# Optimization experiments

Hardware: AMD Instinct MI355X
Metric: run time of the kernel (lower is better)

## Reference

```python
import jax, jax.numpy as jnp
import numpy as np
import math

# ---- static hyperparameters (match init_kwargs) ----
B, N = 128, 2048          # batch, latent tokens per item
IN_DIM, HID = 256, 128    # router input / hidden width
R, MP = 8, 4              # num VQ experts, num phy modes
K, D = 256, 64            # codebook size, code dim
K_BITS = 8                # ceil(log2(K))
BPS = 4                   # bits per symbol -> 16-QAM
MQ = 1 << BPS             # constellation size
TAU = 1.0                 # router temperature
VQ_T = 0.5                # VQ soft-assignment temperature
BIT_T = 0.5               # bit-space mixture temperature
LN_EPS = 1e-5


def _int_to_bits_np(n, num_bits):
    # MSB-first bits of 0..n-1, shape [n, num_bits], float32
    shifts = np.arange(num_bits - 1, -1, -1)
    return ((np.arange(n)[:, None] >> shifts) & 1).astype(np.float32)


def _qam_constellation_np(M):
    # square QAM normalized to max power 1 (matches qam_constellation)
    s = int(math.sqrt(M))
    levels = np.arange(-(s - 1), s + 1, 2).astype(np.float32)
    xs, ys = np.meshgrid(levels, levels, indexing='ij')
    pts = np.stack([xs.reshape(-1), ys.reshape(-1)], axis=-1)
    max_p = (pts ** 2).sum(-1).max()
    return (pts / np.sqrt(max_p + 1e-9)).astype(np.float32)


LABEL_BITS = jnp.asarray(_int_to_bits_np(K, K_BITS))   # [K, 8] identity labeling
CAND_BITS = jnp.asarray(_int_to_bits_np(MQ, BPS))      # [16, 4]
CONST = jnp.asarray(_qam_constellation_np(MQ))         # [16, 2]
POWER = jnp.asarray(np.array([0.25, 0.5, 0.75, 1.0], dtype=np.float32))  # per phy mode


def setup_inputs() -> dict:
    key = jax.random.key(0)
    ks = jax.random.split(key, 10)
    s = 0.02
    return {
        'phi': jax.random.normal(ks[0], (B, IN_DIM), jnp.float32),
        'z': jax.random.normal(ks[1], (B, N, D), jnp.float32),
        'ln_gamma': jnp.ones((IN_DIM,), jnp.float32),
        'ln_beta': jnp.zeros((IN_DIM,), jnp.float32),
        'W1': jax.random.normal(ks[2], (IN_DIM, HID), jnp.float32) * s,
        'b1': jnp.zeros((HID,), jnp.float32),
        'W2': jax.random.normal(ks[3], (HID, HID), jnp.float32) * s,
        'b2': jnp.zeros((HID,), jnp.float32),
        'We': jax.random.normal(ks[4], (HID, R), jnp.float32) * s,
        'be': jnp.zeros((R,), jnp.float32),
        'Wm': jax.random.normal(ks[5], (HID, MP), jnp.float32) * s,
        'bm': jnp.zeros((MP,), jnp.float32),
        'codebooks': jax.random.normal(ks[6], (R, K, D), jnp.float32) * s,
    }


def reference(phi, z, ln_gamma, ln_beta, W1, b1, W2, b2, We, be, Wm, bm, codebooks):
    # ---- ModeRouter: LayerNorm -> MLP(GELU) -> expert/phy heads ----
    mu = phi.mean(-1, keepdims=True)
    var = ((phi - mu) ** 2).mean(-1, keepdims=True)
    x = (phi - mu) * jax.lax.rsqrt(var + LN_EPS) * ln_gamma + ln_beta
    h = jax.nn.gelu(x @ W1 + b1, approximate=False)
    h = jax.nn.gelu(h @ W2 + b2, approximate=False)
    logits_e = h @ We + be                      # [B, R]
    logits_m = h @ Wm + bm                      # [B, MP]
    p_m = jax.nn.softmax(logits_m / TAU, axis=-1)

    # ---- hard expert selection -> per-sample codebook gather ----
    expert_idx = jnp.argmax(logits_e, axis=-1)  # [B]
    cb = codebooks[expert_idx]                  # [B, K, D]

    # ---- VQ distances + soft assignment (dominant memory traffic) ----
    d = (jnp.sum(z ** 2, -1, keepdims=True)
         - 2.0 * jnp.einsum('bnd,bkd->bnk', z, cb)
         + jnp.sum(cb ** 2, -1)[:, None, :])    # [B, N, K]
    soft_assign = jax.nn.softmax(-d / VQ_T, axis=-1)

    # ---- soft code labels -> soft bits -> symbols ----
    soft_bits = jnp.einsum('bnk,kc->bnc', soft_assign, LABEL_BITS)  # [B, N, 8]
    sb = soft_bits.reshape(B, N * K_BITS // BPS, BPS)               # [B, S, 4]
    dist = jnp.sum((sb[..., None, :] - CAND_BITS) ** 2, -1)         # [B, S, 16]
    w_sym = jax.nn.softmax(-dist / BIT_T, axis=-1)
    x_sym = jnp.einsum('bsm,mc->bsc', w_sym, CONST)                 # [B, S, 2]

    # ---- soft phy-mode power blending ----
    scale = p_m @ POWER                                             # [B]
    return x_sym * scale[:, None, None]
```

## Files before the change

kernel.cpp:

```cpp
#include <hip/hip_runtime.h>

typedef __bf16 bf16;
typedef bf16 bf16x8 __attribute__((ext_vector_type(8)));
typedef float f32x4 __attribute__((ext_vector_type(4)));

#define NB    128
#define NTOK  2048
#define INDIM 256
#define HIDW  128
#define NEXP  8
#define NMODE 4
#define KC    256
#define DC    64
#define NSYM  4096
#define TPBK  2

#define RLN2_4 5.770780163555853f
#define RLN2_2 2.8853900817779268f
#define NLN2_8 0.0866433975699932f

__global__ __launch_bounds__(256)
void router_kernel(const float* __restrict__ phi,
                   const float* __restrict__ ln_g, const float* __restrict__ ln_b,
                   const float* __restrict__ W1, const float* __restrict__ b1,
                   const float* __restrict__ W2, const float* __restrict__ b2,
                   const float* __restrict__ We, const float* __restrict__ be,
                   const float* __restrict__ Wm, const float* __restrict__ bm,
                   float* __restrict__ scale_out, int* __restrict__ eidx_out)
{
  const int b = blockIdx.x, t = threadIdx.x;
  __shared__ double xs[INDIM];
  __shared__ double hs[HIDW];
  __shared__ double part[2][HIDW];
  __shared__ double red4[4];
  __shared__ double lg[NEXP + NMODE];

  double v = (double)phi[b * INDIM + t];
  double s = v;
  #pragma unroll
  for (int off = 32; off; off >>= 1) s += __shfl_down(s, off);
  if ((t & 63) == 0) red4[t >> 6] = s;
  __syncthreads();
  double mu = (red4[0] + red4[1] + red4[2] + red4[3]) * (1.0 / 256.0);
  double dv = v - mu;
  double s2 = dv * dv;
  #pragma unroll
  for (int off = 32; off; off >>= 1) s2 += __shfl_down(s2, off);
  __syncthreads();
  if ((t & 63) == 0) red4[t >> 6] = s2;
  __syncthreads();
  double var = (red4[0] + red4[1] + red4[2] + red4[3]) * (1.0 / 256.0);
  xs[t] = dv * (1.0 / sqrt(var + 1e-5)) * (double)ln_g[t] + (double)ln_b[t];
  __syncthreads();

  const int n = t & 127, h = t >> 7;

  {
    double a0 = 0.0, a1 = 0.0;
    const int i0 = h * 128;
    #pragma unroll 4
    for (int i = 0; i < 128; i += 2) {
      a0 += xs[i0 + i]     * (double)W1[(i0 + i)     * HIDW + n];
      a1 += xs[i0 + i + 1] * (double)W1[(i0 + i + 1) * HIDW + n];
    }
    part[h][n] = a0 + a1;
  }
  __syncthreads();
  if (h == 0) {
    double a = part[0][n] + part[1][n] + (double)b1[n];
    hs[n] = a * 0.5 * (1.0 + erf(a * 0.70710678118654752440));
  }
  __syncthreads();

  {
    double a0 = 0.0, a1 = 0.0;
    const int i0 = h * 64;
    #pragma unroll 4
    for (int i = 0; i < 64; i += 2) {
      a0 += hs[i0 + i]     * (double)W2[(i0 + i)     * HIDW + n];
      a1 += hs[i0 + i + 1] * (double)W2[(i0 + i + 1) * HIDW + n];
    }
    part[h][n] = a0 + a1;
  }
  __syncthreads();
  double h2v = 0.0;
  if (h == 0) {
    double a = part[0][n] + part[1][n] + (double)b2[n];
    h2v = a * 0.5 * (1.0 + erf(a * 0.70710678118654752440));
  }
  __syncthreads();
  if (h == 0) part[0][n] = h2v;
  __syncthreads();

  if (t < 192) {
    const int g = t >> 4, j = t & 15;
    const float* W; int stride, col; double bias;
    if (g < NEXP) { W = We; stride = NEXP;  col = g;        bias = (double)be[g]; }
    else          { W = Wm; stride = NMODE; col = g - NEXP; bias = (double)bm[g - NEXP]; }
    double a = 0.0;
    #pragma unroll
    for (int i = 0; i < 8; ++i)
      a += part[0][j * 8 + i] * (double)W[(j * 8 + i) * stride + col];
    a += __shfl_down(a, 8);
    a += __shfl_down(a, 4);
    a += __shfl_down(a, 2);
    a += __shfl_down(a, 1);
    if (j == 0) lg[g] = a + bias;
  }
  __syncthreads();
  if (t == 0) {
    int best = 0; double bv = lg[0];
    for (int j = 1; j < NEXP; ++j) if (lg[j] > bv) { bv = lg[j]; best = j; }
    eidx_out[b] = best;
    double m = lg[NEXP];
    for (int j = 1; j < NMODE; ++j) m = fmax(m, lg[NEXP + j]);
    double den = 0.0, num = 0.0;
    for (int j = 0; j < NMODE; ++j) {
      double e = exp(lg[NEXP + j] - m);
      den += e; num += e * (0.25 * (j + 1));
    }
    scale_out[b] = (float)(num / den);
  }
}

__global__ __launch_bounds__(256, 3)
void vq_kernel(const float* __restrict__ z, const float* __restrict__ codebooks,
               const float* __restrict__ scale_arr, const int* __restrict__ eidx,
               float* __restrict__ out)
{
  __shared__ __align__(16) bf16 cb_s[KC * DC];
  __shared__ float cn2h_s[KC];
  __shared__ __align__(16) float sb_s[4][32 * 8];

  const int blk  = blockIdx.x;
  const int b    = blk >> 3;
  const int tg   = blk & 7;
  const int tid  = threadIdx.x;
  const int lane = tid & 63;
  const int wid  = tid >> 6;
  const int q    = lane >> 4;
  const int c    = lane & 15;

  {
    const int e = eidx[b];
    const float* __restrict__ src = codebooks + (size_t)e * KC * DC + tid * DC;
    char* dstrow = (char*)cb_s + tid * 128;
    const int sw = tid & 7;
    float nrm = 0.f;
    #pragma unroll
    for (int j = 0; j < 8; ++j) {
      float4 va = *(const float4*)(src + j * 8);
      float4 vb = *(const float4*)(src + j * 8 + 4);
      bf16x8 p;
      p[0] = (bf16)(va.x * RLN2_4); p[1] = (bf16)(va.y * RLN2_4);
      p[2] = (bf16)(va.z * RLN2_4); p[3] = (bf16)(va.w * RLN2_4);
      p[4] = (bf16)(vb.x * RLN2_4); p[5] = (bf16)(vb.y * RLN2_4);
      p[6] = (bf16)(vb.z * RLN2_4); p[7] = (bf16)(vb.w * RLN2_4);
      #pragma unroll
      for (int u = 0; u < 8; ++u) { float f = (float)p[u]; nrm += f * f; }
      *(bf16x8*)(dstrow + ((j ^ sw) * 16)) = p;
    }
    cn2h_s[tid] = -NLN2_8 * nrm;
  }
  const float scale_b = scale_arr[b];
  __syncthreads();

  const char* pa0 = (const char*)cb_s + c * 128 + ((q    ) ^ (c & 7)) * 16;
  const char* pa1 = (const char*)cb_s + c * 128 + ((q + 4) ^ (c & 7)) * 16;
  const float* __restrict__ cn2q = cn2h_s + q * 4;

  for (int tile = 0; tile < TPBK; ++tile) {
    const int tokw = tg * (TPBK * 128) + tile * 128 + wid * 32;

    bf16x8 zb[2][2];
    #pragma unroll
    for (int nt = 0; nt < 2; ++nt) {
      const float* __restrict__ zt = z + ((size_t)b * NTOK + tokw + nt * 16 + c) * DC + q * 8;
      #pragma unroll
      for (int ks = 0; ks < 2; ++ks) {
        float4 va = *(const float4*)(zt + ks * 32);
        float4 vb = *(const float4*)(zt + ks * 32 + 4);
        bf16x8 p;
        p[0] = (bf16)va.x; p[1] = (bf16)va.y; p[2] = (bf16)va.z; p[3] = (bf16)va.w;
        p[4] = (bf16)vb.x; p[5] = (bf16)vb.y; p[6] = (bf16)vb.z; p[7] = (bf16)vb.w;
        zb[nt][ks] = p;
      }
    }

    float E[2]  = {0.f, 0.f}, S0[2] = {0.f, 0.f}, S1[2] = {0.f, 0.f},
          S2[2] = {0.f, 0.f}, S3[2] = {0.f, 0.f}, R0[2] = {0.f, 0.f}, R1[2] = {0.f, 0.f};
    #pragma unroll
    for (int cc = 0; cc < 4; ++cc) {
      #pragma unroll
      for (int ci = 0; ci < 4; ++ci) {
        const int ct = cc * 4 + ci;
        f32x4 cinit = *(const f32x4*)(cn2q + ct * 16);
        bf16x8 a0 = *(const bf16x8*)(pa0 + ct * 2048);
        bf16x8 a1 = *(const bf16x8*)(pa1 + ct * 2048);
        #pragma unroll
        for (int nt = 0; nt < 2; ++nt) {
          f32x4 a = __builtin_amdgcn_mfma_f32_16x16x32_bf16(a0, zb[nt][0], cinit, 0, 0, 0);
          a = __builtin_amdgcn_mfma_f32_16x16x32_bf16(a1, zb[nt][1], a, 0, 0, 0);
          float e0 = __builtin_amdgcn_exp2f(a[0]);
          float e1 = __builtin_amdgcn_exp2f(a[1]);
          float e2 = __builtin_amdgcn_exp2f(a[2]);
          float e3 = __builtin_amdgcn_exp2f(a[3]);
          float s01 = e0 + e1, s23 = e2 + e3, g = s01 + s23;
          E[nt] += g; R0[nt] += s23; R1[nt] += e1 + e3;
          if (ct & 8) S0[nt] += g;
          if (ct & 4) S1[nt] += g;
          if (ct & 2) S2[nt] += g;
          if (ct & 1) S3[nt] += g;
        }
      }
      __builtin_amdgcn_sched_barrier(0);
    }

    #pragma unroll
    for (int nt = 0; nt < 2; ++nt) {
      float En = E[nt];
      float Ep = En + __shfl_xor(En, 16);
      float B5 = En + __shfl_xor(En, 32);
      float Et = Ep + __shfl_xor(Ep, 32);
      float s0 = S0[nt], s1 = S1[nt], s2 = S2[nt], s3 = S3[nt], r0 = R0[nt], r1 = R1[nt];
      #define BF2(x) x += __shfl_xor(x, 16); x += __shfl_xor(x, 32);
      BF2(s0) BF2(s1) BF2(s2) BF2(s3) BF2(r0) BF2(r1)
      #undef BF2
      const float rinv = __builtin_amdgcn_rcpf(Et);

      float* row = &sb_s[wid][(nt * 16 + c) * 8];
      float v1 = (q == 0) ? s0 : (q == 1) ? s1 : (q == 2) ? s2 : s3;
      float v2 = (q == 0) ? r0 : (q == 1) ? B5 : (q == 2) ? Ep : r1;
      const int p2 = (q == 3) ? 7 : (6 - q);
      row[q]  = v1 * rinv;
      row[p2] = v2 * rinv;
    }

    {
      const int tok = lane >> 1, sym = lane & 1;
      const float* sb = &sb_s[wid][tok * 8 + sym * 4];
      float u0 = sb[0], u1 = sb[1], u2 = sb[2], u3 = sb[3];
      float wsum = 0.f, xa = 0.f, ya = 0.f;
      #pragma unroll
      for (int m = 0; m < 16; ++m) {
        float su = 0.f;
        if (m & 8) su += u0;
        if (m & 4) su += u1;
        if (m & 2) su += u2;
        if (m & 1) su += u3;
        const float pc = (float)__builtin_popcount(m);
        float ev = __builtin_amdgcn_exp2f(su * RLN2_4 - pc * RLN2_2);
        wsum += ev;
        xa += ev * (float)(2 * (m >> 2) - 3);
        ya += ev * (float)(2 * (m & 3) - 3);
      }
      const float fac = scale_b * 0.23570226039551584f * __builtin_amdgcn_rcpf(wsum);
      const int nidx = tokw + tok;
      float2* op = (float2*)(out + (((size_t)b * NSYM) + 2 * (size_t)nidx + sym) * 2);
      *op = make_float2(xa * fac, ya * fac);
    }
  }
}

extern "C" void kernel_launch(void* const* d_in, const int* in_sizes, int n_in,
                              void* d_out, int out_size, void* d_ws, size_t ws_size,
                              hipStream_t stream) {
  const float* phi  = (const float*)d_in[0];
  const float* z    = (const float*)d_in[1];
  const float* ln_g = (const float*)d_in[2];
  const float* ln_b = (const float*)d_in[3];
  const float* W1   = (const float*)d_in[4];
  const float* b1   = (const float*)d_in[5];
  const float* W2   = (const float*)d_in[6];
  const float* b2   = (const float*)d_in[7];
  const float* We   = (const float*)d_in[8];
  const float* be   = (const float*)d_in[9];
  const float* Wm   = (const float*)d_in[10];
  const float* bm   = (const float*)d_in[11];
  const float* cbk  = (const float*)d_in[12];
  float* out   = (float*)d_out;
  float* scale = (float*)d_ws;
  int*   eidx  = (int*)((char*)d_ws + 512);

  router_kernel<<<NB, 256, 0, stream>>>(phi, ln_g, ln_b, W1, b1, W2, b2,
                                        We, be, Wm, bm, scale, eidx);
  vq_kernel<<<NB * 8, 256, 0, stream>>>(z, cbk, scale, eidx, out);
}
```

Measured before the change: 143.1 us.

## Stage codebook in two halves to halve LDS and double VQ grid

The VQ kernel now holds only half of the codebook (128 codes) in shared memory at a time. It sweeps the first half, syncs, restages the second half, and sweeps again, with the bit-0 accumulation driven by which half is loaded. Each block handles one 128-token tile instead of two, and the grid grows from 1024 to 2048 blocks. The aim is lower LDS use per block, so more blocks fit per CU and there is more parallelism. The cost is that each block stages the codebook from global memory, converts it and syncs twice, and total codebook staging work per batch doubles.

```diff
diff --git a/kernel.cpp b/kernel.cpp
--- a/kernel.cpp
+++ b/kernel.cpp
@@ -11,9 +11,9 @@
 #define NEXP  8
 #define NMODE 4
 #define KC    256
+#define KH    128
 #define DC    64
 #define NSYM  4096
-#define TPBK  2
 
 #define RLN2_4 5.770780163555853f
 #define RLN2_2 2.8853900817779268f
@@ -123,142 +123,161 @@
   }
 }
 
+__device__ __forceinline__ void stage_half(int half, int tid, int e,
+                                           const float* __restrict__ codebooks,
+                                           bf16* cb_s, float* cn2h_s)
+{
+  const int code = tid >> 1, prt = tid & 1;
+  const float* __restrict__ src = codebooks + (size_t)e * KC * DC
+                                + (size_t)(half * KH + code) * DC + prt * 32;
+  char* dstrow = (char*)cb_s + code * 128;
+  const int sw = code & 7;
+  float nrm = 0.f;
+  #pragma unroll
+  for (int j2 = 0; j2 < 4; ++j2) {
+    const int j = prt * 4 + j2;
+    float4 va = *(const float4*)(src + j2 * 8);
+    float4 vb = *(const float4*)(src + j2 * 8 + 4);
+    bf16x8 p;
+    p[0] = (bf16)(va.x * RLN2_4); p[1] = (bf16)(va.y * RLN2_4);
+    p[2] = (bf16)(va.z * RLN2_4); p[3] = (bf16)(va.w * RLN2_4);
+    p[4] = (bf16)(vb.x * RLN2_4); p[5] = (bf16)(vb.y * RLN2_4);
+    p[6] = (bf16)(vb.z * RLN2_4); p[7] = (bf16)(vb.w * RLN2_4);
+    #pragma unroll
+    for (int u = 0; u < 8; ++u) { float f = (float)p[u]; nrm += f * f; }
+    *(bf16x8*)(dstrow + ((j ^ sw) * 16)) = p;
+  }
+  nrm += __shfl_xor(nrm, 1);
+  if (prt == 0) cn2h_s[code] = -NLN2_8 * nrm;
+}
+
 __global__ __launch_bounds__(256, 3)
 void vq_kernel(const float* __restrict__ z, const float* __restrict__ codebooks,
                const float* __restrict__ scale_arr, const int* __restrict__ eidx,
                float* __restrict__ out)
 {
-  __shared__ __align__(16) bf16 cb_s[KC * DC];
-  __shared__ float cn2h_s[KC];
+  __shared__ __align__(16) bf16 cb_s[KH * DC];
+  __shared__ float cn2h_s[KH];
   __shared__ __align__(16) float sb_s[4][32 * 8];
 
   const int blk  = blockIdx.x;
-  const int b    = blk >> 3;
-  const int tg   = blk & 7;
+  const int b    = blk >> 4;
+  const int tg   = blk & 15;
   const int tid  = threadIdx.x;
   const int lane = tid & 63;
   const int wid  = tid >> 6;
   const int q    = lane >> 4;
   const int c    = lane & 15;
 
-  {
-    const int e = eidx[b];
-    const float* __restrict__ src = codebooks + (size_t)e * KC * DC + tid * DC;
-    char* dstrow = (char*)cb_s + tid * 128;
-    const int sw = tid & 7;
-    float nrm = 0.f;
-    #pragma unroll
-    for (int j = 0; j < 8; ++j) {
-      float4 va = *(const float4*)(src + j * 8);
-      float4 vb = *(const float4*)(src + j * 8 + 4);
-      bf16x8 p;
-      p[0] = (bf16)(va.x * RLN2_4); p[1] = (bf16)(va.y * RLN2_4);
-      p[2] = (bf16)(va.z * RLN2_4); p[3] = (bf16)(va.w * RLN2_4);
-      p[4] = (bf16)(vb.x * RLN2_4); p[5] = (bf16)(vb.y * RLN2_4);
-      p[6] = (bf16)(vb.z * RLN2_4); p[7] = (bf16)(vb.w * RLN2_4);
-      #pragma unroll
-      for (int u = 0; u < 8; ++u) { float f = (float)p[u]; nrm += f * f; }
-      *(bf16x8*)(dstrow + ((j ^ sw) * 16)) = p;
-    }
-    cn2h_s[tid] = -NLN2_8 * nrm;
-  }
+  const int e = eidx[b];
   const float scale_b = scale_arr[b];
+
+  stage_half(0, tid, e, codebooks, cb_s, cn2h_s);
   __syncthreads();
 
   const char* pa0 = (const char*)cb_s + c * 128 + ((q    ) ^ (c & 7)) * 16;
   const char* pa1 = (const char*)cb_s + c * 128 + ((q + 4) ^ (c & 7)) * 16;
   const float* __restrict__ cn2q = cn2h_s + q * 4;
 
-  for (int tile = 0; tile < TPBK; ++tile) {
-    const int tokw = tg * (TPBK * 128) + tile * 128 + wid * 32;
-
-    bf16x8 zb[2][2];
+  const int tokw = tg * 128 + wid * 32;
+
+  bf16x8 zb[2][2];
+  #pragma unroll
+  for (int nt = 0; nt < 2; ++nt) {
+    const float* __restrict__ zt = z + ((size_t)b * NTOK + tokw + nt * 16 + c) * DC + q * 8;
     #pragma unroll
-    for (int nt = 0; nt < 2; ++nt) {
-      const float* __restrict__ zt = z + ((size_t)b * NTOK + tokw + nt * 16 + c) * DC + q * 8;
-      #pragma unroll
-      for (int ks = 0; ks < 2; ++ks) {
-        float4 va = *(const float4*)(zt + ks * 32);
-        float4 vb = *(const float4*)(zt + ks * 32 + 4);
-        bf16x8 p;
-        p[0] = (bf16)va.x; p[1] = (bf16)va.y; p[2] = (bf16)va.z; p[3] = (bf16)va.w;
-        p[4] = (bf16)vb.x; p[5] = (bf16)vb.y; p[6] = (bf16)vb.z; p[7] = (bf16)vb.w;
-        zb[nt][ks] = p;
-      }
-    }
-
-    float E[2]  = {0.f, 0.f}, S0[2] = {0.f, 0.f}, S1[2] = {0.f, 0.f},
-          S2[2] = {0.f, 0.f}, S3[2] = {0.f, 0.f}, R0[2] = {0.f, 0.f}, R1[2] = {0.f, 0.f};
+    for (int ks = 0; ks < 2; ++ks) {
+      float4 va = *(const float4*)(zt + ks * 32);
+      float4 vb = *(const float4*)(zt + ks * 32 + 4);
+      bf16x8 p;
+      p[0] = (bf16)va.x; p[1] = (bf16)va.y; p[2] = (bf16)va.z; p[3] = (bf16)va.w;
+      p[4] = (bf16)vb.x; p[5] = (bf16)vb.y; p[6] = (bf16)vb.z; p[7] = (bf16)vb.w;
+      zb[nt][ks] = p;
+    }
+  }
+
+  float E[2]  = {0.f, 0.f}, S0[2] = {0.f, 0.f}, S1[2] = {0.f, 0.f},
+        S2[2] = {0.f, 0.f}, S3[2] = {0.f, 0.f}, R0[2] = {0.f, 0.f}, R1[2] = {0.f, 0.f};
+
+#define SWEEP(HALFBIT) \
+  _Pragma("unroll") \
+  for (int cc = 0; cc < 2; ++cc) { \
+    _Pragma("unroll") \
+    for (int ci = 0; ci < 4; ++ci) { \
+      const int ct = cc * 4 + ci; \
+      f32x4 cinit = *(const f32x4*)(cn2q + ct * 16); \
+      bf16x8 a0 = *(const bf16x8*)(pa0 + ct * 2048); \
+      bf16x8 a1 = *(const bf16x8*)(pa1 + ct * 2048); \
+      _Pragma("unroll") \
+      for (int nt = 0; nt < 2; ++nt) { \
+        f32x4 a = __builtin_amdgcn_mfma_f32_16x16x32_bf16(a0, zb[nt][0], cinit, 0, 0, 0); \
+        a = __builtin_amdgcn_mfma_f32_16x16x32_bf16(a1, zb[nt][1], a, 0, 0, 0); \
+        float e0 = __builtin_amdgcn_exp2f(a[0]); \
+        float e1 = __builtin_amdgcn_exp2f(a[1]); \
+        float e2 = __builtin_amdgcn_exp2f(a[2]); \
+        float e3 = __builtin_amdgcn_exp2f(a[3]); \
+        float s01 = e0 + e1, s23 = e2 + e3, g = s01 + s23; \
+        E[nt] += g; R0[nt] += s23; R1[nt] += e1 + e3; \
+        if (HALFBIT) S0[nt] += g; \
+        if (ct & 4) S1[nt] += g; \
+        if (ct & 2) S2[nt] += g; \
+        if (ct & 1) S3[nt] += g; \
+      } \
+    } \
+    __builtin_amdgcn_sched_barrier(0);  \
+  }
+
+  SWEEP(0)
+
+  __syncthreads();
+  stage_half(1, tid, e, codebooks, cb_s, cn2h_s);
+  __syncthreads();
+
+  SWEEP(1)
+#undef SWEEP
+
+  #pragma unroll
+  for (int nt = 0; nt < 2; ++nt) {
+    float En = E[nt];
+    float Ep = En + __shfl_xor(En, 16);
+    float B5 = En + __shfl_xor(En, 32);
+    float Et = Ep + __shfl_xor(Ep, 32);
+    float s0 = S0[nt], s1 = S1[nt], s2 = S2[nt], s3 = S3[nt], r0 = R0[nt], r1 = R1[nt];
+    #define BF2(x) x += __shfl_xor(x, 16); x += __shfl_xor(x, 32);
+    BF2(s0) BF2(s1) BF2(s2) BF2(s3) BF2(r0) BF2(r1)
+    #undef BF2
+    const float rinv = __builtin_amdgcn_rcpf(Et);
+
+    float* row = &sb_s[wid][(nt * 16 + c) * 8];
+    float v1 = (q == 0) ? s0 : (q == 1) ? s1 : (q == 2) ? s2 : s3;
+    float v2 = (q == 0) ? r0 : (q == 1) ? B5 : (q == 2) ? Ep : r1;
+    const int p2 = (q == 3) ? 7 : (6 - q);
+    row[q]  = v1 * rinv;
+    row[p2] = v2 * rinv;
+  }
+
+  {
+    const int tok = lane >> 1, sym = lane & 1;
+    const float* sb = &sb_s[wid][tok * 8 + sym * 4];
+    float u0 = sb[0], u1 = sb[1], u2 = sb[2], u3 = sb[3];
+    float wsum = 0.f, xa = 0.f, ya = 0.f;
     #pragma unroll
-    for (int cc = 0; cc < 4; ++cc) {
-      #pragma unroll
-      for (int ci = 0; ci < 4; ++ci) {
-        const int ct = cc * 4 + ci;
-        f32x4 cinit = *(const f32x4*)(cn2q + ct * 16);
-        bf16x8 a0 = *(const bf16x8*)(pa0 + ct * 2048);
-        bf16x8 a1 = *(const bf16x8*)(pa1 + ct * 2048);
-        #pragma unroll
-        for (int nt = 0; nt < 2; ++nt) {
-          f32x4 a = __builtin_amdgcn_mfma_f32_16x16x32_bf16(a0, zb[nt][0], cinit, 0, 0, 0);
-          a = __builtin_amdgcn_mfma_f32_16x16x32_bf16(a1, zb[nt][1], a, 0, 0, 0);
-          float e0 = __builtin_amdgcn_exp2f(a[0]);
-          float e1 = __builtin_amdgcn_exp2f(a[1]);
-          float e2 = __builtin_amdgcn_exp2f(a[2]);
-          float e3 = __builtin_amdgcn_exp2f(a[3]);
-          float s01 = e0 + e1, s23 = e2 + e3, g = s01 + s23;
-          E[nt] += g; R0[nt] += s23; R1[nt] += e1 + e3;
-          if (ct & 8) S0[nt] += g;
-          if (ct & 4) S1[nt] += g;
-          if (ct & 2) S2[nt] += g;
-          if (ct & 1) S3[nt] += g;
-        }
-      }
-      __builtin_amdgcn_sched_barrier(0);
-    }
-
-    #pragma unroll
-    for (int nt = 0; nt < 2; ++nt) {
-      float En = E[nt];
-      float Ep = En + __shfl_xor(En, 16);
-      float B5 = En + __shfl_xor(En, 32);
-      float Et = Ep + __shfl_xor(Ep, 32);
-      float s0 = S0[nt], s1 = S1[nt], s2 = S2[nt], s3 = S3[nt], r0 = R0[nt], r1 = R1[nt];
-      #define BF2(x) x += __shfl_xor(x, 16); x += __shfl_xor(x, 32);
-      BF2(s0) BF2(s1) BF2(s2) BF2(s3) BF2(r0) BF2(r1)
-      #undef BF2
-      const float rinv = __builtin_amdgcn_rcpf(Et);
-
-      float* row = &sb_s[wid][(nt * 16 + c) * 8];
-      float v1 = (q == 0) ? s0 : (q == 1) ? s1 : (q == 2) ? s2 : s3;
-      float v2 = (q == 0) ? r0 : (q == 1) ? B5 : (q == 2) ? Ep : r1;
-      const int p2 = (q == 3) ? 7 : (6 - q);
-      row[q]  = v1 * rinv;
-      row[p2] = v2 * rinv;
-    }
-
-    {
-      const int tok = lane >> 1, sym = lane & 1;
-      const float* sb = &sb_s[wid][tok * 8 + sym * 4];
-      float u0 = sb[0], u1 = sb[1], u2 = sb[2], u3 = sb[3];
-      float wsum = 0.f, xa = 0.f, ya = 0.f;
-      #pragma unroll
-      for (int m = 0; m < 16; ++m) {
-        float su = 0.f;
-        if (m & 8) su += u0;
-        if (m & 4) su += u1;
-        if (m & 2) su += u2;
-        if (m & 1) su += u3;
-        const float pc = (float)__builtin_popcount(m);
-        float ev = __builtin_amdgcn_exp2f(su * RLN2_4 - pc * RLN2_2);
-        wsum += ev;
-        xa += ev * (float)(2 * (m >> 2) - 3);
-        ya += ev * (float)(2 * (m & 3) - 3);
-      }
-      const float fac = scale_b * 0.23570226039551584f * __builtin_amdgcn_rcpf(wsum);
-      const int nidx = tokw + tok;
-      float2* op = (float2*)(out + (((size_t)b * NSYM) + 2 * (size_t)nidx + sym) * 2);
-      *op = make_float2(xa * fac, ya * fac);
-    }
+    for (int m = 0; m < 16; ++m) {
+      float su = 0.f;
+      if (m & 8) su += u0;
+      if (m & 4) su += u1;
+      if (m & 2) su += u2;
+      if (m & 1) su += u3;
+      const float pc = (float)__builtin_popcount(m);
+      float ev = __builtin_amdgcn_exp2f(su * RLN2_4 - pc * RLN2_2);
+      wsum += ev;
+      xa += ev * (float)(2 * (m >> 2) - 3);
+      ya += ev * (float)(2 * (m & 3) - 3);
+    }
+    const float fac = scale_b * 0.23570226039551584f * __builtin_amdgcn_rcpf(wsum);
+    const int nidx = tokw + tok;
+    float2* op = (float2*)(out + (((size_t)b * NSYM) + 2 * (size_t)nidx + sym) * 2);
+    *op = make_float2(xa * fac, ya * fac);
   }
 }
 
@@ -284,5 +303,5 @@
 
   router_kernel<<<NB, 256, 0, stream>>>(phi, ln_g, ln_b, W1, b1, W2, b2,
                                         We, be, Wm, bm, scale, eidx);
-  vq_kernel<<<NB * 8, 256, 0, stream>>>(z, cbk, scale, eidx, out);
+  vq_kernel<<<NB * 16, 256, 0, stream>>>(z, cbk, scale, eidx, out);
 }
```

After: 150.6 us. 1.05x slower.
